# Kernel optimization log

Measured on AMD Instinct MI355X. Metric: run time of the kernel, lower is better.

Reference implementation:

```python
import jax, jax.numpy as jnp
import numpy as np

D_MODEL = 2048
N_HEADS = 16
HEAD_DIM = D_MODEL // N_HEADS
BATCH = 2
SEQ = 2048


def rotate_half(x):
    x1, x2 = jnp.split(x, 2, axis=-1)
    return jnp.concatenate((-x2, x1), axis=-1)


def rope_emb(seq_len, head_dim, dtype=jnp.float32):
    inv_freq = 1.0 / (10000.0 ** (jnp.arange(0, head_dim, 2, dtype=jnp.float32) / head_dim))
    t = jnp.arange(seq_len, dtype=jnp.float32)
    freqs = jnp.einsum('i,j->ij', t, inv_freq)            # [S, D/2]
    emb = jnp.concatenate((freqs, freqs), axis=-1)        # [S, D]
    return emb[None, :, None, :].astype(dtype)            # [1, S, 1, D]


def apply_rope(x, emb):
    return x * jnp.cos(emb) + rotate_half(x) * jnp.sin(emb)


def setup_inputs() -> dict:
    key = jax.random.key(0)
    ks = jax.random.split(key, 5)
    s = 1.0 / np.sqrt(D_MODEL)
    return {
        'query': jax.random.normal(ks[0], (BATCH, SEQ, D_MODEL), jnp.float32),
        'Wq': jax.random.normal(ks[1], (D_MODEL, D_MODEL), jnp.float32) * s,
        'Wk': jax.random.normal(ks[2], (D_MODEL, D_MODEL), jnp.float32) * s,
        'Wv': jax.random.normal(ks[3], (D_MODEL, D_MODEL), jnp.float32) * s,
        'Wo': jax.random.normal(ks[4], (D_MODEL, D_MODEL), jnp.float32) * s,
    }


def reference(query, Wq, Wk, Wv, Wo):
    B, S, _ = query.shape
    # QKV projections (nn.Linear: x @ W.T), reshape to [B, S, H, Dh]
    q = (query @ Wq.T).reshape(B, S, N_HEADS, HEAD_DIM)
    k = (query @ Wk.T).reshape(B, S, N_HEADS, HEAD_DIM)
    v = (query @ Wv.T).reshape(B, S, N_HEADS, HEAD_DIM)
    emb = rope_emb(S, HEAD_DIM, q.dtype)
    q = apply_rope(q, emb)
    k = apply_rope(k, emb)
    # causal SDPA
    scale = HEAD_DIM ** -0.5
    scores = jnp.einsum('bqhd,bkhd->bhqk', q, k) * scale  # [B, H, S, S]
    causal = jnp.tril(jnp.ones((S, S), dtype=bool))
    scores = jnp.where(causal, scores, jnp.finfo(scores.dtype).min)
    attn = jax.nn.softmax(scores, axis=-1)
    out = jnp.einsum('bhqk,bkhd->bqhd', attn, v).reshape(B, S, D_MODEL)
    return out @ Wo.T
```

## Files before the change

kernel.cpp:

```cpp
#include <hip/hip_runtime.h>
#include <math.h>

#define BATCH 2
#define SEQ 2048
#define DMODEL 2048
#define NHEADS 16
#define HEADDIM 128
#define MTOT (BATCH * SEQ)
#define QKVLD 6144

typedef __attribute__((ext_vector_type(8))) _Float16 half8;
typedef __attribute__((ext_vector_type(4))) _Float16 half4;
typedef __attribute__((ext_vector_type(4))) float f32x4;

__device__ __forceinline__ void gl_lds16(const void* g, void* l) {
    __builtin_amdgcn_global_load_lds(
        (const __attribute__((address_space(1))) unsigned int*)g,
        (__attribute__((address_space(3))) unsigned int*)l, 16, 0, 0);
}

__global__ __launch_bounds__(256) void f2h_conv(const float* __restrict__ src,
                                                _Float16* __restrict__ dst) {
    size_t i = ((size_t)blockIdx.x * 256 + threadIdx.x) * 8;
    float4 a = *(const float4*)(src + i);
    float4 b = *(const float4*)(src + i + 4);
    union { uint4 u; _Float16 h[8]; } o;
    o.h[0] = (_Float16)a.x; o.h[1] = (_Float16)a.y;
    o.h[2] = (_Float16)a.z; o.h[3] = (_Float16)a.w;
    o.h[4] = (_Float16)b.x; o.h[5] = (_Float16)b.y;
    o.h[6] = (_Float16)b.z; o.h[7] = (_Float16)b.w;
    *(uint4*)(dst + i) = o.u;
}

__global__ __launch_bounds__(256) void f2h3_conv(const float* __restrict__ s0,
                                                 const float* __restrict__ s1,
                                                 const float* __restrict__ s2,
                                                 _Float16* __restrict__ dst) {
    const float* src = (blockIdx.y == 0) ? s0 : (blockIdx.y == 1) ? s1 : s2;
    size_t i = ((size_t)blockIdx.x * 256 + threadIdx.x) * 8;
    float4 a = *(const float4*)(src + i);
    float4 b = *(const float4*)(src + i + 4);
    union { uint4 u; _Float16 h[8]; } o;
    o.h[0] = (_Float16)a.x; o.h[1] = (_Float16)a.y;
    o.h[2] = (_Float16)a.z; o.h[3] = (_Float16)a.w;
    o.h[4] = (_Float16)b.x; o.h[5] = (_Float16)b.y;
    o.h[6] = (_Float16)b.z; o.h[7] = (_Float16)b.w;
    *(uint4*)(dst + (size_t)blockIdx.y * (DMODEL * DMODEL) + i) = o.u;
}

template <bool F16OUT>
__global__ __launch_bounds__(256) void gemm_h(const _Float16* __restrict__ A,
                                              const _Float16* __restrict__ W,
                                              void* __restrict__ Cout,
                                              int M, int N, int K) {
    __shared__ __align__(16) _Float16 As[128 * 32];
    __shared__ __align__(16) _Float16 Bs[128 * 32];

    const int tid = threadIdx.x;
    const int wv = tid >> 6;
    const int ln = tid & 63;
    const int quad = ln >> 4;
    const int lcol = ln & 15;
    const int m0 = blockIdx.y * 128;
    const int n0 = blockIdx.x * 128;
    const int wm = (wv >> 1) * 64;
    const int wn = (wv & 1) * 64;

    const int srow = ln >> 2;
    const int kblk = (ln & 3) * 8;

    f32x4 acc[4][4];
#pragma unroll
    for (int i = 0; i < 4; i++)
#pragma unroll
        for (int j = 0; j < 4; j++) acc[i][j] = (f32x4){0.f, 0.f, 0.f, 0.f};

    for (int k0 = 0; k0 < K; k0 += 32) {
        __syncthreads();
#pragma unroll
        for (int j = 0; j < 2; j++) {
            int r = wv * 32 + j * 16 + srow;
            gl_lds16(A + (size_t)(m0 + r) * K + k0 + kblk, &As[r * 32 + kblk]);
            gl_lds16(W + (size_t)(n0 + r) * K + k0 + kblk, &Bs[r * 32 + kblk]);
        }
        __syncthreads();

        half8 af[4], bf[4];
#pragma unroll
        for (int ms = 0; ms < 4; ms++)
            af[ms] = *(const half8*)&As[(wm + ms * 16 + lcol) * 32 + quad * 8];
#pragma unroll
        for (int ns = 0; ns < 4; ns++)
            bf[ns] = *(const half8*)&Bs[(wn + ns * 16 + lcol) * 32 + quad * 8];
#pragma unroll
        for (int ms = 0; ms < 4; ms++)
#pragma unroll
            for (int ns = 0; ns < 4; ns++)
                acc[ms][ns] = __builtin_amdgcn_mfma_f32_16x16x32_f16(
                    af[ms], bf[ns], acc[ms][ns], 0, 0, 0);
    }

    float* Cf = (float*)Cout;
    _Float16* Ch = (_Float16*)Cout;
#pragma unroll
    for (int ms = 0; ms < 4; ms++)
#pragma unroll
        for (int ns = 0; ns < 4; ns++)
#pragma unroll
            for (int r = 0; r < 4; r++) {
                size_t row = m0 + wm + ms * 16 + quad * 4 + r;
                size_t col = n0 + wn + ns * 16 + lcol;
                if (F16OUT)
                    Ch[row * N + col] = (_Float16)acc[ms][ns][r];
                else
                    Cf[row * N + col] = acc[ms][ns][r];
            }
}

__global__ __launch_bounds__(256) void rope_qk(_Float16* __restrict__ buf) {
    size_t idx = (size_t)blockIdx.x * 256 + threadIdx.x;
    int d = (int)(idx & 63);
    int h = (int)((idx >> 6) & (NHEADS - 1));
    int qk = (int)((idx >> 10) & 1);
    int m = (int)(idx >> 11);
    int s = m & (SEQ - 1);
    float scale = qk ? 1.0f : 0.08838834764831845f;
    float inv = __expf(-(float)d * 0.14391156831212787f);
    float f = (float)s * inv;
    float sn, cs;
    __sincosf(f, &sn, &cs);
    size_t base = (size_t)m * QKVLD + qk * DMODEL + h * HEADDIM + d;
    float x1 = (float)buf[base];
    float x2 = (float)buf[base + 64];
    buf[base]      = (_Float16)((x1 * cs - x2 * sn) * scale);
    buf[base + 64] = (_Float16)((x2 * cs + x1 * sn) * scale);
}

__global__ __launch_bounds__(256) void conv_v_t(const _Float16* __restrict__ src,
                                                _Float16* __restrict__ dst) {
    __shared__ __align__(16) _Float16 T[32][72];
    const int tid = threadIdx.x;
    const int s0 = blockIdx.x * 64;
    const int d0 = blockIdx.y * 32;
    const int bh = blockIdx.z;
    const int b = bh >> 4;
    const int h = bh & 15;

    {
        int s = tid >> 2;
        int d8 = (tid & 3) * 8;
        union { uint4 u; _Float16 hh[8]; } v;
        v.u = *(const uint4*)(src + (size_t)(b * SEQ + s0 + s) * QKVLD +
                              2 * DMODEL + h * HEADDIM + d0 + d8);
#pragma unroll
        for (int j = 0; j < 8; j++) T[d8 + j][s] = v.hh[j];
    }
    __syncthreads();

    int row = tid >> 3;
    int chunk = tid & 7;
    uint4 val = *(const uint4*)&T[row][chunk * 8];
    *(uint4*)(dst + ((size_t)(bh * HEADDIM + d0 + row)) * SEQ + s0 + chunk * 8) = val;
}

__global__ __launch_bounds__(512) void attn_mfma(const _Float16* __restrict__ qkv,
                                                 const _Float16* __restrict__ vtb,
                                                 _Float16* __restrict__ ab) {
    __shared__ __align__(16) _Float16 Ks[64][136];
    __shared__ __align__(16) _Float16 Vts[128][72];
    __shared__ __align__(16) _Float16 Ps[8][16][72];

    const int tid = threadIdx.x;
    const int wave = tid >> 6;
    const int lane = tid & 63;
    const int quad = lane >> 4;
    const int lcol = lane & 15;

    const int h = blockIdx.y;
    const int b = blockIdx.z;
    const int qtA = blockIdx.x;

    const int kr0 = tid >> 4;
    const int ko0 = (tid & 15) * 8;
    const int vr0 = tid >> 3;
    const int vo0 = (tid & 7) * 8;

    const _Float16* kbp = qkv + (size_t)b * SEQ * QKVLD + DMODEL + h * HEADDIM;
    const _Float16* vbp = vtb + ((size_t)(b * NHEADS + h) * HEADDIM) * SEQ;

    uint4 kA, kB, vA, vB;
#define ISSUE_LOAD(kb)                                                        \
    do {                                                                      \
        int _kb = (kb);                                                       \
        kA = *(const uint4*)(kbp + (size_t)(_kb + kr0) * QKVLD + ko0);        \
        kB = *(const uint4*)(kbp + (size_t)(_kb + 32 + kr0) * QKVLD + ko0);   \
        vA = *(const uint4*)(vbp + (size_t)vr0 * SEQ + _kb + vo0);            \
        vB = *(const uint4*)(vbp + (size_t)(vr0 + 64) * SEQ + _kb + vo0);     \
    } while (0)

    ISSUE_LOAD(0);

    for (int ph = 0; ph < 2; ++ph) {
        const int qt = ph ? (15 - qtA) : qtA;
        const int q0 = qt * 128 + wave * 16;
        const int nkt = 2 * qt + 2;

        half8 aq[4];
        {
            const _Float16* qrow =
                qkv + (size_t)(b * SEQ + q0 + lcol) * QKVLD + h * HEADDIM;
#pragma unroll
            for (int st = 0; st < 4; st++)
                aq[st] = *(const half8*)(qrow + quad * 8 + 32 * st);
        }

        f32x4 Of[8];
#pragma unroll
        for (int dt = 0; dt < 8; dt++) Of[dt] = (f32x4){0.f, 0.f, 0.f, 0.f};
        float m_s = -1e30f, l_s = 0.f;

        for (int kt = 0; kt < nkt; ++kt) {
            const int kbase = kt << 6;

            __syncthreads();
            *(uint4*)&Ks[kr0][ko0]        = kA;
            *(uint4*)&Ks[kr0 + 32][ko0]   = kB;
            *(uint4*)&Vts[vr0][vo0]       = vA;
            *(uint4*)&Vts[vr0 + 64][vo0]  = vB;
            __syncthreads();

            if (kt + 1 < nkt)      ISSUE_LOAD((kt + 1) << 6);
            else if (ph == 0)      ISSUE_LOAD(0);

            if (kbase > q0 + 15) continue;

            f32x4 Sc[4];
#pragma unroll
            for (int s = 0; s < 4; s++) {
                Sc[s] = (f32x4){0.f, 0.f, 0.f, 0.f};
#pragma unroll
                for (int st = 0; st < 4; st++) {
                    half8 bk = *(const half8*)&Ks[16 * s + lcol][quad * 8 + 32 * st];
                    Sc[s] = __builtin_amdgcn_mfma_f32_16x16x32_f16(bk, aq[st], Sc[s],
                                                                   0, 0, 0);
                }
            }

            if (kbase + 63 > q0) {
#pragma unroll
                for (int s = 0; s < 4; s++)
#pragma unroll
                    for (int r = 0; r < 4; r++)
                        if (kbase + 16 * s + quad * 4 + r > q0 + lcol)
                            Sc[s][r] = -1e30f;
            }

            float pmax = Sc[0][0];
#pragma unroll
            for (int s = 0; s < 4; s++)
#pragma unroll
                for (int r = 0; r < 4; r++) pmax = fmaxf(pmax, Sc[s][r]);
            pmax = fmaxf(pmax, __shfl_xor(pmax, 16));
            pmax = fmaxf(pmax, __shfl_xor(pmax, 32));

            if (!__all(pmax <= m_s + 5.0f)) {
                float mnew = fmaxf(m_s, pmax);
                float alpha = __expf(m_s - mnew);
                m_s = mnew;
                l_s *= alpha;
                float a0 = __shfl(alpha, quad * 4 + 0);
                float a1 = __shfl(alpha, quad * 4 + 1);
                float a2 = __shfl(alpha, quad * 4 + 2);
                float a3 = __shfl(alpha, quad * 4 + 3);
#pragma unroll
                for (int dt = 0; dt < 8; dt++) {
                    Of[dt][0] *= a0;
                    Of[dt][1] *= a1;
                    Of[dt][2] *= a2;
                    Of[dt][3] *= a3;
                }
            }

            float sum = 0.f;
#pragma unroll
            for (int s = 0; s < 4; s++)
#pragma unroll
                for (int r = 0; r < 4; r++) {
                    float p = __expf(Sc[s][r] - m_s);
                    Sc[s][r] = p;
                    sum += p;
                }
            sum += __shfl_xor(sum, 16);
            sum += __shfl_xor(sum, 32);
            l_s += sum;

#pragma unroll
            for (int s = 0; s < 4; s++) {
                union { half4 v; unsigned long long u; } pk;
                pk.v[0] = (_Float16)Sc[s][0];
                pk.v[1] = (_Float16)Sc[s][1];
                pk.v[2] = (_Float16)Sc[s][2];
                pk.v[3] = (_Float16)Sc[s][3];
                *(half4*)&Ps[wave][lcol][16 * s + 4 * quad] = pk.v;
            }

            half8 ap[2];
#pragma unroll
            for (int st = 0; st < 2; st++)
                ap[st] = *(const half8*)&Ps[wave][lcol][quad * 8 + 32 * st];
#pragma unroll
            for (int dt = 0; dt < 8; dt++) {
#pragma unroll
                for (int st = 0; st < 2; st++) {
                    half8 bv = *(const half8*)&Vts[16 * dt + lcol][quad * 8 + 32 * st];
                    Of[dt] = __builtin_amdgcn_mfma_f32_16x16x32_f16(ap[st], bv, Of[dt],
                                                                    0, 0, 0);
                }
            }
        }

        float invl = 1.f / l_s;
        float i0 = __shfl(invl, quad * 4 + 0);
        float i1 = __shfl(invl, quad * 4 + 1);
        float i2 = __shfl(invl, quad * 4 + 2);
        float i3 = __shfl(invl, quad * 4 + 3);
        _Float16* obase =
            ab + (size_t)(b * SEQ + q0 + quad * 4) * DMODEL + h * HEADDIM;
#pragma unroll
        for (int dt = 0; dt < 8; dt++) {
            obase[(size_t)0 * DMODEL + 16 * dt + lcol] = (_Float16)(Of[dt][0] * i0);
            obase[(size_t)1 * DMODEL + 16 * dt + lcol] = (_Float16)(Of[dt][1] * i1);
            obase[(size_t)2 * DMODEL + 16 * dt + lcol] = (_Float16)(Of[dt][2] * i2);
            obase[(size_t)3 * DMODEL + 16 * dt + lcol] = (_Float16)(Of[dt][3] * i3);
        }
    }
#undef ISSUE_LOAD
}

extern "C" void kernel_launch(void* const* d_in, const int* in_sizes, int n_in,
                              void* d_out, int out_size, void* d_ws, size_t ws_size,
                              hipStream_t stream) {
    const float* query = (const float*)d_in[0];
    const float* Wq = (const float*)d_in[1];
    const float* Wk = (const float*)d_in[2];
    const float* Wv = (const float*)d_in[3];
    const float* Wo = (const float*)d_in[4];
    float* out = (float*)d_out;

    const size_t MB = 1024 * 1024;
    char* w = (char*)d_ws;
    _Float16* xh   = (_Float16*)(w + 0 * MB);
    _Float16* ab   = (_Float16*)(w + 0 * MB);
    _Float16* qkvh = (_Float16*)(w + 16 * MB);
    _Float16* Wh3  = (_Float16*)(w + 64 * MB);
    _Float16* vtb  = (_Float16*)(w + 88 * MB);

    const int convX = (MTOT * DMODEL) / (256 * 8);
    const int convW = (DMODEL * DMODEL) / (256 * 8);
    const int ropeBlocks = (MTOT * 2 * NHEADS * 64) / 256;

    f2h_conv<<<convX, 256, 0, stream>>>(query, xh);
    f2h3_conv<<<dim3(convW, 3), 256, 0, stream>>>(Wq, Wk, Wv, Wh3);

    gemm_h<true><<<dim3(QKVLD / 128, MTOT / 128), 256, 0, stream>>>(
        xh, Wh3, qkvh, MTOT, QKVLD, DMODEL);

    rope_qk<<<ropeBlocks, 256, 0, stream>>>(qkvh);
    conv_v_t<<<dim3(SEQ / 64, HEADDIM / 32, BATCH * NHEADS), 256, 0, stream>>>(qkvh, vtb);

    attn_mfma<<<dim3(8, NHEADS, BATCH), 512, 0, stream>>>(qkvh, vtb, ab);

    f2h_conv<<<convW, 256, 0, stream>>>(Wo, Wh3);
    gemm_h<false><<<dim3(DMODEL / 128, MTOT / 128), 256, 0, stream>>>(
        ab, Wh3, out, MTOT, DMODEL, DMODEL);
}
```

Before: 441.7 us.

## Replace projection GEMMs with 256x256 double-buffered swizzled 8-wave pipelined kernel

Replaces the simple 128x128 single-buffered GEMM with a 256x256 tile kernel that uses 8 waves, double-buffered LDS with an XOR swizzle, and manual s_barrier/vmcnt scheduling. Global-to-LDS loads for the next k-tiles are interleaved between MFMA phases, and setprio raises priority around the compute phases. The aim is to hide memory latency, get more data reuse per tile, and avoid LDS bank conflicts. In exchange it uses much more LDS (128KB), more accumulator registers, and fewer blocks (fewer tiles for the output GEMM), which may cause tail or occupancy problems.

```diff
diff --git a/kernel.cpp b/kernel.cpp
--- a/kernel.cpp
+++ b/kernel.cpp
@@ -48,73 +48,156 @@
     *(uint4*)(dst + (size_t)blockIdx.y * (DMODEL * DMODEL) + i) = o.u;
 }
 
+#define GBAR asm volatile("s_barrier" ::: "memory")
+#define VM4  asm volatile("s_waitcnt vmcnt(4)" ::: "memory")
+#define VM0  asm volatile("s_waitcnt vmcnt(0)" ::: "memory")
+
 template <bool F16OUT>
-__global__ __launch_bounds__(256) void gemm_h(const _Float16* __restrict__ A,
-                                              const _Float16* __restrict__ W,
-                                              void* __restrict__ Cout,
-                                              int M, int N, int K) {
-    __shared__ __align__(16) _Float16 As[128 * 32];
-    __shared__ __align__(16) _Float16 Bs[128 * 32];
+__global__ __launch_bounds__(512, 2) void gemm8p(const _Float16* __restrict__ A,
+                                                 const _Float16* __restrict__ W,
+                                                 void* __restrict__ Cout,
+                                                 int M, int N, int K) {
+    __shared__ __align__(16) _Float16 LAb[2][2][128][64];
+    __shared__ __align__(16) _Float16 LBb[2][2][128][64];
 
     const int tid = threadIdx.x;
-    const int wv = tid >> 6;
-    const int ln = tid & 63;
-    const int quad = ln >> 4;
-    const int lcol = ln & 15;
-    const int m0 = blockIdx.y * 128;
-    const int n0 = blockIdx.x * 128;
-    const int wm = (wv >> 1) * 64;
-    const int wn = (wv & 1) * 64;
-
-    const int srow = ln >> 2;
-    const int kblk = (ln & 3) * 8;
-
-    f32x4 acc[4][4];
-#pragma unroll
-    for (int i = 0; i < 4; i++)
+    const int lane = tid & 63;
+    const int wave = tid >> 6;
+    const int quad = lane >> 4;
+    const int lcol = lane & 15;
+    const int wr = wave >> 2;
+    const int wc = wave & 3;
+    const int m0 = blockIdx.y * 256;
+    const int n0 = blockIdx.x * 256;
+
+    const int srow = tid >> 3;
+    const int sc8p = tid & 7;
+    const int sc8l = sc8p ^ (srow & 7);
+
+#define STA(BUF, HALF, KT)                                                     \
+    do {                                                                       \
+        _Pragma("unroll") for (int j = 0; j < 2; j++)                          \
+            gl_lds16(A + (size_t)(m0 + (HALF)*128 + j*64 + srow) * K +         \
+                         (KT)*64 + sc8l*8,                                     \
+                     &LAb[BUF][HALF][j*64 + srow][sc8p*8]);                    \
+    } while (0)
+#define STB(BUF, HALF, KT)                                                     \
+    do {                                                                       \
+        _Pragma("unroll") for (int j = 0; j < 2; j++)                          \
+            gl_lds16(W + (size_t)(n0 + (HALF)*128 + j*64 + srow) * K +         \
+                         (KT)*64 + sc8l*8,                                     \
+                     &LBb[BUF][HALF][j*64 + srow][sc8p*8]);                    \
+    } while (0)
+
+    auto rdA = [&](int buf, int mf, int ks) -> half8 {
+        int R = mf * 16 + lcol;
+        return *(const half8*)&LAb[buf][wr][R]
+                [(ks * 32 + quad * 8) ^ ((lcol & 7) << 3)];
+    };
+    auto rdB = [&](int buf, int nf, int ks) -> half8 {
+        int R = (wc & 1) * 64 + nf * 16 + lcol;
+        return *(const half8*)&LBb[buf][wc >> 1][R]
+                [(ks * 32 + quad * 8) ^ ((lcol & 7) << 3)];
+    };
+
+    f32x4 acc[8][4];
+#pragma unroll
+    for (int i = 0; i < 8; i++)
 #pragma unroll
         for (int j = 0; j < 4; j++) acc[i][j] = (f32x4){0.f, 0.f, 0.f, 0.f};
 
-    for (int k0 = 0; k0 < K; k0 += 32) {
-        __syncthreads();
-#pragma unroll
-        for (int j = 0; j < 2; j++) {
-            int r = wv * 32 + j * 16 + srow;
-            gl_lds16(A + (size_t)(m0 + r) * K + k0 + kblk, &As[r * 32 + kblk]);
-            gl_lds16(W + (size_t)(n0 + r) * K + k0 + kblk, &Bs[r * 32 + kblk]);
-        }
-        __syncthreads();
-
-        half8 af[4], bf[4];
-#pragma unroll
-        for (int ms = 0; ms < 4; ms++)
-            af[ms] = *(const half8*)&As[(wm + ms * 16 + lcol) * 32 + quad * 8];
-#pragma unroll
-        for (int ns = 0; ns < 4; ns++)
-            bf[ns] = *(const half8*)&Bs[(wn + ns * 16 + lcol) * 32 + quad * 8];
-#pragma unroll
-        for (int ms = 0; ms < 4; ms++)
-#pragma unroll
-            for (int ns = 0; ns < 4; ns++)
-                acc[ms][ns] = __builtin_amdgcn_mfma_f32_16x16x32_f16(
-                    af[ms], bf[ns], acc[ms][ns], 0, 0, 0);
+#define KTILE4(BUF, S1, S2, S3, S4, W4)                                        \
+    {                                                                          \
+        half8 a[4][2], b[4][2];                                                \
+                         \
+        _Pragma("unroll") for (int mf = 0; mf < 4; mf++)                       \
+            _Pragma("unroll") for (int ks = 0; ks < 2; ks++)                   \
+                a[mf][ks] = rdA(BUF, mf, ks);                                  \
+        _Pragma("unroll") for (int nf = 0; nf < 2; nf++)                       \
+            _Pragma("unroll") for (int ks = 0; ks < 2; ks++)                   \
+                b[nf][ks] = rdB(BUF, nf, ks);                                  \
+        S1; GBAR;                                                              \
+        __builtin_amdgcn_s_setprio(1);                                         \
+        _Pragma("unroll") for (int ks = 0; ks < 2; ks++)                       \
+            _Pragma("unroll") for (int mf = 0; mf < 4; mf++)                   \
+                _Pragma("unroll") for (int nf = 0; nf < 2; nf++)               \
+                    acc[mf][nf] = __builtin_amdgcn_mfma_f32_16x16x32_f16(      \
+                        a[mf][ks], b[nf][ks], acc[mf][nf], 0, 0, 0);           \
+        __builtin_amdgcn_s_setprio(0); GBAR;                                   \
+                                             \
+        _Pragma("unroll") for (int nf = 0; nf < 2; nf++)                       \
+            _Pragma("unroll") for (int ks = 0; ks < 2; ks++)                   \
+                b[2 + nf][ks] = rdB(BUF, 2 + nf, ks);                          \
+        S2; GBAR;                                                              \
+        __builtin_amdgcn_s_setprio(1);                                         \
+        _Pragma("unroll") for (int ks = 0; ks < 2; ks++)                       \
+            _Pragma("unroll") for (int mf = 0; mf < 4; mf++)                   \
+                _Pragma("unroll") for (int nf = 0; nf < 2; nf++)               \
+                    acc[mf][2 + nf] = __builtin_amdgcn_mfma_f32_16x16x32_f16(  \
+                        a[mf][ks], b[2 + nf][ks], acc[mf][2 + nf], 0, 0, 0);   \
+        __builtin_amdgcn_s_setprio(0); GBAR;                                   \
+               \
+        _Pragma("unroll") for (int mf = 0; mf < 4; mf++)                       \
+            _Pragma("unroll") for (int ks = 0; ks < 2; ks++)                   \
+                a[mf][ks] = rdA(BUF, 4 + mf, ks);                              \
+        S3; GBAR;                                                              \
+        __builtin_amdgcn_s_setprio(1);                                         \
+        _Pragma("unroll") for (int ks = 0; ks < 2; ks++)                       \
+            _Pragma("unroll") for (int mf = 0; mf < 4; mf++)                   \
+                _Pragma("unroll") for (int nf = 0; nf < 2; nf++)               \
+                    acc[4 + mf][nf] = __builtin_amdgcn_mfma_f32_16x16x32_f16(  \
+                        a[mf][ks], b[nf][ks], acc[4 + mf][nf], 0, 0, 0);       \
+        __builtin_amdgcn_s_setprio(0); GBAR;                                   \
+                                                 \
+        S4; W4; GBAR;                                                          \
+        __builtin_amdgcn_s_setprio(1);                                         \
+        _Pragma("unroll") for (int ks = 0; ks < 2; ks++)                       \
+            _Pragma("unroll") for (int mf = 0; mf < 4; mf++)                   \
+                _Pragma("unroll") for (int nf = 0; nf < 2; nf++)               \
+                    acc[4 + mf][2 + nf] =                                      \
+                        __builtin_amdgcn_mfma_f32_16x16x32_f16(                \
+                            a[mf][ks], b[2 + nf][ks], acc[4 + mf][2 + nf],     \
+                            0, 0, 0);                                          \
+        __builtin_amdgcn_s_setprio(0); GBAR;                                   \
+    }
+
+    STB(0, 0, 0); STB(0, 1, 0); STA(0, 0, 0); STA(0, 1, 0);
+    STB(1, 0, 1); STB(1, 1, 1);
+    VM4; GBAR;
+
+    const int niter = K >> 7;
+    for (int i = 0; i < niter - 1; ++i) {
+        const int t0 = 2 * i;
+        KTILE4(0, STA(1, 0, t0 + 1), STA(1, 1, t0 + 1),
+                  STB(0, 0, t0 + 2), STB(0, 1, t0 + 2), VM4);
+        KTILE4(1, STA(0, 0, t0 + 2), STA(0, 1, t0 + 2),
+                  STB(1, 0, t0 + 3), STB(1, 1, t0 + 3), VM4);
+    }
+    {
+        const int t0 = 2 * (niter - 1);
+        KTILE4(0, STA(1, 0, t0 + 1), STA(1, 1, t0 + 1),
+                  (void)0, (void)0, VM0);
+        KTILE4(1, (void)0, (void)0, (void)0, (void)0, (void)0);
     }
 
     float* Cf = (float*)Cout;
     _Float16* Ch = (_Float16*)Cout;
 #pragma unroll
-    for (int ms = 0; ms < 4; ms++)
-#pragma unroll
-        for (int ns = 0; ns < 4; ns++)
+    for (int mf = 0; mf < 8; mf++)
+#pragma unroll
+        for (int nf = 0; nf < 4; nf++)
 #pragma unroll
             for (int r = 0; r < 4; r++) {
-                size_t row = m0 + wm + ms * 16 + quad * 4 + r;
-                size_t col = n0 + wn + ns * 16 + lcol;
+                size_t row = m0 + wr * 128 + mf * 16 + quad * 4 + r;
+                size_t col = n0 + wc * 64 + nf * 16 + lcol;
                 if (F16OUT)
-                    Ch[row * N + col] = (_Float16)acc[ms][ns][r];
+                    Ch[row * N + col] = (_Float16)acc[mf][nf][r];
                 else
-                    Cf[row * N + col] = acc[ms][ns][r];
-            }
+                    Cf[row * N + col] = acc[mf][nf][r];
+            }
+#undef KTILE4
+#undef STA
+#undef STB
 }
 
 __global__ __launch_bounds__(256) void rope_qk(_Float16* __restrict__ buf) {
@@ -362,7 +445,7 @@
     f2h_conv<<<convX, 256, 0, stream>>>(query, xh);
     f2h3_conv<<<dim3(convW, 3), 256, 0, stream>>>(Wq, Wk, Wv, Wh3);
 
-    gemm_h<true><<<dim3(QKVLD / 128, MTOT / 128), 256, 0, stream>>>(
+    gemm8p<true><<<dim3(QKVLD / 256, MTOT / 256), 512, 0, stream>>>(
         xh, Wh3, qkvh, MTOT, QKVLD, DMODEL);
 
     rope_qk<<<ropeBlocks, 256, 0, stream>>>(qkvh);
@@ -371,6 +454,6 @@
     attn_mfma<<<dim3(8, NHEADS, BATCH), 512, 0, stream>>>(qkvh, vtb, ab);
 
     f2h_conv<<<convW, 256, 0, stream>>>(Wo, Wh3);
-    gemm_h<false><<<dim3(DMODEL / 128, MTOT / 128), 256, 0, stream>>>(
+    gemm8p<false><<<dim3(DMODEL / 256, MTOT / 256), 512, 0, stream>>>(
         ab, Wh3, out, MTOT, DMODEL, DMODEL);
 }
```

Result: no change. 439.0 us (-0.6%).
